# Performance work log

Hardware: AMD Instinct MI355X
Metric: run time of the kernel (lower is better)

## Reference

```python
import jax, jax.numpy as jnp
import numpy as np

ALPHA = 0.25        # focal alpha
GAMMA = 2.0         # focal gamma
POS_T = 0.5         # max_iou positive threshold
NEG_T = 0.4         # max_iou negative threshold
SL1_BETA = 1.0 / 9.0  # smooth_l1 with sigma=3
EPS = 1e-6

N, T, A, C = 8, 64, 65536, 80


def setup_inputs() -> dict:
    key = jax.random.key(0)
    ks = jax.random.split(key, 6)
    labels = jax.random.randint(ks[0], (N, T), 1, C)
    y_true = jax.nn.one_hot(labels, C, dtype=jnp.float32)
    xy = jax.random.uniform(ks[1], (N, T, 2)) * 0.7
    wh = jax.random.uniform(ks[2], (N, T, 2)) * 0.25 + 0.02
    bbox_true = jnp.concatenate([xy, xy + wh], axis=-1)
    valid = (jnp.arange(T) < 24).astype(jnp.float32)  # zero-pad remaining GT rows
    bbox_true = bbox_true * valid[None, :, None]
    axy = jax.random.uniform(ks[3], (A, 2)) * 0.9
    awh = jax.random.uniform(jax.random.fold_in(ks[3], 1), (A, 2)) * 0.15 + 0.02
    anchors = jnp.concatenate([axy, axy + awh], axis=-1)
    y_pred = jax.random.normal(ks[4], (N, A, C), dtype=jnp.float32)
    bbox_pred = jax.random.normal(ks[5], (N, A, 4), dtype=jnp.float32) * 0.1
    return {"y_true": y_true, "bbox_true": bbox_true, "y_pred": y_pred,
            "bbox_pred": bbox_pred, "anchors": anchors}


def _iou(b1, b2):
    # b1: (T,4), b2: (A,4) -> (T,A)
    a1 = jnp.maximum(b1[:, 2] - b1[:, 0], 0) * jnp.maximum(b1[:, 3] - b1[:, 1], 0)
    a2 = jnp.maximum(b2[:, 2] - b2[:, 0], 0) * jnp.maximum(b2[:, 3] - b2[:, 1], 0)
    lt = jnp.maximum(b1[:, None, :2], b2[None, :, :2])
    rb = jnp.minimum(b1[:, None, 2:], b2[None, :, 2:])
    wh = jnp.maximum(rb - lt, 0.0)
    inter = wh[..., 0] * wh[..., 1]
    union = a1[:, None] + a2[None, :] - inter
    return inter / jnp.maximum(union, 1e-10)


def _bbox2delta(boxes, anchors):
    # standard (dx, dy, dw, dh) encoding, mean=0 / std=1
    wa = jnp.maximum(anchors[:, 2] - anchors[:, 0], EPS)
    ha = jnp.maximum(anchors[:, 3] - anchors[:, 1], EPS)
    cxa = anchors[:, 0] + 0.5 * wa
    cya = anchors[:, 1] + 0.5 * ha
    wt = jnp.maximum(boxes[:, 2] - boxes[:, 0], EPS)
    ht = jnp.maximum(boxes[:, 3] - boxes[:, 1], EPS)
    cxt = boxes[:, 0] + 0.5 * (boxes[:, 2] - boxes[:, 0])
    cyt = boxes[:, 1] + 0.5 * (boxes[:, 3] - boxes[:, 1])
    return jnp.stack([(cxt - cxa) / wa, (cyt - cya) / ha,
                      jnp.log(wt / wa), jnp.log(ht / ha)], axis=-1)


def _encode_target(y_true_i, bbox_true_i, anchors):
    # y_true_i: (T,C), bbox_true_i: (T,4), anchors: (A,4)
    valid = jnp.any(bbox_true_i > 0, axis=-1)                 # (T,)
    iou = jnp.where(valid[:, None], _iou(bbox_true_i, anchors), -1.0)  # (T,A)
    max_iou = iou.max(axis=0)                                  # (A,)
    assigned = iou.argmax(axis=0)                              # (A,) gt index per anchor
    pos = max_iou >= POS_T
    neg = (max_iou < NEG_T)
    # low-quality matching: each valid gt's best anchor is positive for that gt
    gt_best = iou.argmax(axis=1)                               # (T,)
    gt_best_iou = iou.max(axis=1)
    lq = valid & (gt_best_iou > 0)
    assigned = assigned.at[gt_best].set(jnp.where(lq, jnp.arange(bbox_true_i.shape[0]), assigned[gt_best]))
    pos = pos.at[gt_best].set(jnp.where(lq, True, pos[gt_best]))
    neg = neg & (~pos)
    state = jnp.where(pos, 1, jnp.where(neg, -1, 0)).astype(jnp.int8)[:, None]  # (A,1)
    # class target: background one-hot [1,0,...,0], positives get gt label
    bg = jnp.zeros((anchors.shape[0], y_true_i.shape[-1]), jnp.float32).at[:, 0].set(1.0)
    yt = jnp.where(pos[:, None], y_true_i[assigned], bg)       # (A,C)
    delta = _bbox2delta(bbox_true_i[assigned], anchors)        # (A,4)
    bt = jnp.where(pos[:, None], delta, 0.0)
    return state, yt, bt


def _focal_bce(y_true, logits):
    # elementwise sigmoid focal loss
    ce = jnp.maximum(logits, 0) - logits * y_true + jnp.log1p(jnp.exp(-jnp.abs(logits)))
    p = jax.nn.sigmoid(logits)
    p_t = y_true * p + (1.0 - y_true) * (1.0 - p)
    a_t = y_true * ALPHA + (1.0 - y_true) * (1.0 - ALPHA)
    return a_t * jnp.power(1.0 - p_t, GAMMA) * ce


def _smooth_l1(y_true, y_pred):
    d = jnp.abs(y_true - y_pred)
    return jnp.where(d < SL1_BETA, 0.5 * d * d / SL1_BETA, d - 0.5 * SL1_BETA)


def _sanitize(x):
    return jnp.where(jnp.isnan(x) | jnp.isinf(x), 0.0, x)


def reference(y_true, bbox_true, y_pred, bbox_pred, anchors):
    state, yt, bt = jax.vmap(lambda a, b: _encode_target(a, b, anchors))(y_true, bbox_true)
    positive_w = (state == 1).astype(y_pred.dtype)   # (N,A,1)
    target_w = (state != 0).astype(y_pred.dtype)     # (N,A,1)
    avg_factor = jnp.sum(jnp.maximum(jnp.sum(positive_w, axis=-2), 1.0))
    yt = yt * positive_w                              # background=False zeroes non-positives
    cls = jnp.sum(_focal_bce(yt, y_pred) * target_w) / avg_factor
    box = jnp.sum(_smooth_l1(bt, bbox_pred) * positive_w) / avg_factor
    return _sanitize(cls), _sanitize(box)
```

## Files before the change

kernel.cpp:

```cpp
#include <hip/hip_runtime.h>
#include <hip/hip_bf16.h>
#include <math.h>

#define NB 8
#define TB 64
#define AB 65536
#define CB 80
#define EPSF 1e-6f

#define LOSS_BLOCKS 2048
#define LOSS_ITERS  16

#define WS_LABEL_OFF  4096
#define WS_CODE_OFF   8192
#define WS_PCLS_OFF   (WS_CODE_OFF + NB*AB*4)
#define WS_PBOX_OFF   (WS_PCLS_OFF + LOSS_BLOCKS*4)
#define WS_PPOS_OFF   (WS_PBOX_OFF + LOSS_BLOCKS*4)

__device__ __forceinline__ float focal0(float l) {
    float u  = __expf(l);
    float r  = __builtin_amdgcn_rcpf(1.f + u);
    float p  = 1.f - r;
    float lg = __log2f(r);
    return p * p * lg * -0.5198603854f;
}
__device__ __forceinline__ float focal_diff(float l) {
    float u  = __expf(l);
    float r  = __builtin_amdgcn_rcpf(1.f + u);
    float p  = 1.f - r;
    float sp = -0.6931471806f * __log2f(r);
    float f1 = 0.25f * r * r * (sp - l);
    float f0 = 0.75f * p * p * sp;
    return f1 - f0;
}
__device__ __forceinline__ float smooth_l1(float x) {
    float d = fabsf(x);
    return d < (1.f / 9.f) ? 4.5f * d * d : d - (0.5f / 9.f);
}

__global__ __launch_bounds__(256) void assign_kernel(
    const float* __restrict__ bbox_true,
    const float* __restrict__ anchors,
    int*   __restrict__ code,
    unsigned long long* __restrict__ gt_key)
{
    __shared__ float4 s_box[TB];
    __shared__ float  s_a1[TB];
    __shared__ unsigned long long s_key[TB];

    const int blk   = blockIdx.x;
    const int i     = blk >> 8;
    const int abase = (blk & 255) << 8;
    const int tid   = threadIdx.x;

    if (tid < TB) {
        float4 b = ((const float4*)bbox_true)[i * TB + tid];
        s_box[tid] = b;
        s_a1[tid]  = fmaxf(b.z - b.x, 0.f) * fmaxf(b.w - b.y, 0.f);
        s_key[tid] = 0ull;
    }
    __syncthreads();

    const int a = abase + tid;
    const float4 an = ((const float4*)anchors)[a];
    const float a2 = fmaxf(an.z - an.x, 0.f) * fmaxf(an.w - an.y, 0.f);

    float best = -1.0f;
    int bestt = 0;
    #pragma unroll 8
    for (int t = 0; t < TB; ++t) {
        float4 b = s_box[t];
        float lx = fmaxf(b.x, an.x), ly = fmaxf(b.y, an.y);
        float rx = fminf(b.z, an.z), ry = fminf(b.w, an.w);
        float w = fmaxf(rx - lx, 0.f), h = fmaxf(ry - ly, 0.f);
        float inter = w * h;
        float uni = s_a1[t] + a2 - inter;
        float iou = inter * __builtin_amdgcn_rcpf(fmaxf(uni, 1e-10f));
        if (iou > 0.f) {
            unsigned long long key =
                ((unsigned long long)__float_as_uint(iou) << 32) |
                (unsigned long long)((unsigned)a ^ 0xFFFFFFFFu);
            if (key > s_key[t])
                atomicMax(&s_key[t], key);
        }
        if (iou > best) { best = iou; bestt = t; }
    }
    bool pos = best >= 0.5f;
    bool neg = best < 0.4f;
    code[i * AB + a] = pos ? bestt : (neg ? -1 : -2);

    __syncthreads();
    if (tid < TB) {
        unsigned long long k = s_key[tid];
        if (k) atomicMax(&gt_key[i * TB + tid], k);
    }
}

__global__ void lq_label_kernel(const unsigned long long* __restrict__ gt_key,
                                const float* __restrict__ y_true,
                                int* __restrict__ code,
                                int* __restrict__ labels)
{
    __shared__ unsigned long long sk[NB * TB];
    const int tid = threadIdx.x;
    sk[tid] = gt_key[tid];

    const float* row = y_true + (size_t)tid * CB;
    int lab = 0;
    for (int c = 0; c < CB; ++c)
        if (row[c] > 0.5f) lab = c;
    labels[tid] = lab;

    __syncthreads();
    const int i = tid >> 6, t = tid & 63;
    unsigned long long k = sk[tid];
    if (k) {
        unsigned a = (unsigned)(k & 0xFFFFFFFFull) ^ 0xFFFFFFFFu;
        bool win = true;
        for (int t2 = t + 1; t2 < TB; ++t2) {
            unsigned long long k2 = sk[(i << 6) | t2];
            if (k2 && (((unsigned)(k2 & 0xFFFFFFFFull) ^ 0xFFFFFFFFu) == a))
                win = false;
        }
        if (win) code[i * AB + (int)a] = t;
    }
}

__global__ __launch_bounds__(320) void loss_kernel(
    const float* __restrict__ bbox_true,
    const float* __restrict__ y_pred,
    const float* __restrict__ bbox_pred,
    const float* __restrict__ anchors,
    const int*   __restrict__ code,
    const int*   __restrict__ labels,
    float* __restrict__ partial_cls,
    float* __restrict__ partial_box,
    int*   __restrict__ partial_pos)
{
    const int tid   = threadIdx.x;
    const int la    = tid / 20;
    const int chunk = tid % 20;
    const int b   = blockIdx.x;
    const int i   = b >> 8;
    const int sub = b & 255;

    const float4* yp4 = (const float4*)y_pred;

    float cls_acc = 0.f, box_acc = 0.f;
    int posc = 0;

    #pragma unroll 2
    for (int it = 0; it < LOSS_ITERS; ++it) {
        const int a = sub * 16 + la + it * (256 * 16);
        const int g = i * AB + a;
        const int cv = code[g];
        float4 l4 = yp4[g * 20 + chunk];
        if (cv != -2) {
            cls_acc += focal0(l4.x) + focal0(l4.y) + focal0(l4.z) + focal0(l4.w);
            if (cv >= 0) {
                int lab = labels[i * TB + cv];
                if (chunk == (lab >> 2)) {
                    int e = lab & 3;
                    float le = (e == 0) ? l4.x : (e == 1) ? l4.y
                             : (e == 2) ? l4.z : l4.w;
                    cls_acc += focal_diff(le);
                }
                if (chunk == 0) {
                    posc += 1;
                    float4 bt = ((const float4*)bbox_true)[i * TB + cv];
                    float4 an = ((const float4*)anchors)[a];
                    float wa = fmaxf(an.z - an.x, EPSF), ha = fmaxf(an.w - an.y, EPSF);
                    float cxa = an.x + 0.5f * wa,  cya = an.y + 0.5f * ha;
                    float wt = fmaxf(bt.z - bt.x, EPSF), ht = fmaxf(bt.w - bt.y, EPSF);
                    float cxt = bt.x + 0.5f * (bt.z - bt.x);
                    float cyt = bt.y + 0.5f * (bt.w - bt.y);
                    float d0 = (cxt - cxa) / wa, d1 = (cyt - cya) / ha;
                    float d2 = __logf(wt / wa),  d3 = __logf(ht / ha);
                    float4 bp = ((const float4*)bbox_pred)[g];
                    box_acc += smooth_l1(d0 - bp.x) + smooth_l1(d1 - bp.y) +
                               smooth_l1(d2 - bp.z) + smooth_l1(d3 - bp.w);
                }
            }
        }
    }

    for (int off = 32; off > 0; off >>= 1) {
        cls_acc += __shfl_down(cls_acc, off);
        box_acc += __shfl_down(box_acc, off);
        posc    += __shfl_down(posc, off);
    }
    __shared__ float s_cls[5], s_box[5];
    __shared__ int   s_pc[5];
    int wave = tid >> 6, lane = tid & 63;
    if (lane == 0) { s_cls[wave] = cls_acc; s_box[wave] = box_acc; s_pc[wave] = posc; }
    __syncthreads();
    if (tid == 0) {
        partial_cls[b] = s_cls[0] + s_cls[1] + s_cls[2] + s_cls[3] + s_cls[4];
        partial_box[b] = s_box[0] + s_box[1] + s_box[2] + s_box[3] + s_box[4];
        partial_pos[b] = s_pc[0] + s_pc[1] + s_pc[2] + s_pc[3] + s_pc[4];
    }
}

__global__ __launch_bounds__(256) void reduce_kernel(
    const float* __restrict__ partial_cls,
    const float* __restrict__ partial_box,
    const int*   __restrict__ partial_pos,
    float* __restrict__ out)
{
    const int tid = threadIdx.x;
    const int wave = tid >> 6, lane = tid & 63;
    __shared__ double sc[4], sb[4];
    __shared__ int    si[4];
    __shared__ float  s_avg;

    double c = 0.0, bx = 0.0;
    #pragma unroll
    for (int j = 0; j < LOSS_BLOCKS / 256; ++j) {
        c  += (double)partial_cls[tid + j * 256];
        bx += (double)partial_box[tid + j * 256];
    }

    float avg = 0.f;
    for (int bb = 0; bb < NB; ++bb) {
        int p = partial_pos[bb * 256 + tid];
        for (int off = 32; off > 0; off >>= 1) p += __shfl_down(p, off);
        if (lane == 0) si[wave] = p;
        __syncthreads();
        if (tid == 0) {
            int tot = si[0] + si[1] + si[2] + si[3];
            avg += fmaxf((float)tot, 1.0f);
        }
        __syncthreads();
    }
    if (tid == 0) s_avg = avg;

    for (int off = 32; off > 0; off >>= 1) {
        c  += __shfl_down(c, off);
        bx += __shfl_down(bx, off);
    }
    if (lane == 0) { sc[wave] = c; sb[wave] = bx; }
    __syncthreads();
    if (tid == 0) {
        double ct = sc[0] + sc[1] + sc[2] + sc[3];
        double bt = sb[0] + sb[1] + sb[2] + sb[3];
        float cf = (float)(ct / (double)s_avg);
        float bf = (float)(bt / (double)s_avg);
        if (isnan(cf) || isinf(cf)) cf = 0.f;
        if (isnan(bf) || isinf(bf)) bf = 0.f;
        out[0] = cf;
        out[1] = bf;
    }
}

extern "C" void kernel_launch(void* const* d_in, const int* in_sizes, int n_in,
                              void* d_out, int out_size, void* d_ws, size_t ws_size,
                              hipStream_t stream) {
    const float* y_true    = (const float*)d_in[0];
    const float* bbox_true = (const float*)d_in[1];
    const float* y_pred    = (const float*)d_in[2];
    const float* bbox_pred = (const float*)d_in[3];
    const float* anchors   = (const float*)d_in[4];
    float* out = (float*)d_out;

    char* ws = (char*)d_ws;
    unsigned long long* gt_key = (unsigned long long*)ws;
    int*   labels  = (int*)(ws + WS_LABEL_OFF);
    int*   code    = (int*)(ws + WS_CODE_OFF);
    float* p_cls   = (float*)(ws + WS_PCLS_OFF);
    float* p_box   = (float*)(ws + WS_PBOX_OFF);
    int*   p_pos   = (int*)(ws + WS_PPOS_OFF);

    hipMemsetAsync(ws, 0, 4096, stream);

    assign_kernel<<<NB * AB / 256, 256, 0, stream>>>(bbox_true, anchors, code, gt_key);
    lq_label_kernel<<<1, NB * TB, 0, stream>>>(gt_key, y_true, code, labels);
    loss_kernel<<<LOSS_BLOCKS, 320, 0, stream>>>(
        bbox_true, y_pred, bbox_pred, anchors, code, labels,
        p_cls, p_box, p_pos);
    reduce_kernel<<<1, 256, 0, stream>>>(p_cls, p_box, p_pos, out);
}
```

Measured before the change: 308.4 us.

## Replace per-anchor atomic GT-best tracking with dedicated per-GT reduction kernel

Removes the shared-memory and global 64-bit atomicMax used to find each ground truth's best anchor inside the assign kernel. A new gtbest kernel runs one block per GT box, scans all anchors, and reduces with shuffles, skipping zero-padded GT rows. Because every key is now written directly, the workspace memset is dropped. The loss kernel also applies the ignore mask as a multiply instead of a branch and unrolls deeper. This adds a second full IoU pass over the anchors and one more kernel launch.

```diff
diff --git a/kernel.cpp b/kernel.cpp
--- a/kernel.cpp
+++ b/kernel.cpp
@@ -41,12 +41,10 @@
 __global__ __launch_bounds__(256) void assign_kernel(
     const float* __restrict__ bbox_true,
     const float* __restrict__ anchors,
-    int*   __restrict__ code,
-    unsigned long long* __restrict__ gt_key)
+    int*   __restrict__ code)
 {
     __shared__ float4 s_box[TB];
     __shared__ float  s_a1[TB];
-    __shared__ unsigned long long s_key[TB];
 
     const int blk   = blockIdx.x;
     const int i     = blk >> 8;
@@ -57,7 +55,6 @@
         float4 b = ((const float4*)bbox_true)[i * TB + tid];
         s_box[tid] = b;
         s_a1[tid]  = fmaxf(b.z - b.x, 0.f) * fmaxf(b.w - b.y, 0.f);
-        s_key[tid] = 0ull;
     }
     __syncthreads();
 
@@ -76,23 +73,55 @@
         float inter = w * h;
         float uni = s_a1[t] + a2 - inter;
         float iou = inter * __builtin_amdgcn_rcpf(fmaxf(uni, 1e-10f));
-        if (iou > 0.f) {
-            unsigned long long key =
-                ((unsigned long long)__float_as_uint(iou) << 32) |
-                (unsigned long long)((unsigned)a ^ 0xFFFFFFFFu);
-            if (key > s_key[t])
-                atomicMax(&s_key[t], key);
-        }
         if (iou > best) { best = iou; bestt = t; }
     }
     bool pos = best >= 0.5f;
     bool neg = best < 0.4f;
     code[i * AB + a] = pos ? bestt : (neg ? -1 : -2);
-
-    __syncthreads();
-    if (tid < TB) {
-        unsigned long long k = s_key[tid];
-        if (k) atomicMax(&gt_key[i * TB + tid], k);
+}
+
+__global__ __launch_bounds__(512) void gtbest_kernel(
+    const float* __restrict__ bbox_true,
+    const float* __restrict__ anchors,
+    unsigned long long* __restrict__ gt_key)
+{
+    const int bt  = blockIdx.x;
+    const int tid = threadIdx.x;
+    const float4 b = ((const float4*)bbox_true)[bt];
+    const bool valid = (b.x > 0.f) || (b.y > 0.f) || (b.z > 0.f) || (b.w > 0.f);
+    const float a1 = fmaxf(b.z - b.x, 0.f) * fmaxf(b.w - b.y, 0.f);
+
+    unsigned long long best = 0ull;
+    if (valid) {
+        for (int a = tid; a < AB; a += 512) {
+            float4 an = ((const float4*)anchors)[a];
+            float a2 = fmaxf(an.z - an.x, 0.f) * fmaxf(an.w - an.y, 0.f);
+            float lx = fmaxf(b.x, an.x), ly = fmaxf(b.y, an.y);
+            float rx = fminf(b.z, an.z), ry = fminf(b.w, an.w);
+            float w = fmaxf(rx - lx, 0.f), h = fmaxf(ry - ly, 0.f);
+            float inter = w * h;
+            float uni = a1 + a2 - inter;
+            float iou = inter * __builtin_amdgcn_rcpf(fmaxf(uni, 1e-10f));
+            unsigned long long key = (iou > 0.f)
+                ? (((unsigned long long)__float_as_uint(iou) << 32) |
+                   (unsigned long long)((unsigned)a ^ 0xFFFFFFFFu))
+                : 0ull;
+            best = (key > best) ? key : best;
+        }
+    }
+    for (int off = 32; off > 0; off >>= 1) {
+        unsigned long long o = __shfl_down(best, off);
+        best = (o > best) ? o : best;
+    }
+    __shared__ unsigned long long sk[8];
+    int wave = tid >> 6, lane = tid & 63;
+    if (lane == 0) sk[wave] = best;
+    __syncthreads();
+    if (tid == 0) {
+        unsigned long long m = sk[0];
+        #pragma unroll
+        for (int wv = 1; wv < 8; ++wv) m = (sk[wv] > m) ? sk[wv] : m;
+        gt_key[bt] = m;
     }
 }
 
@@ -140,46 +169,45 @@
     const int tid   = threadIdx.x;
     const int la    = tid / 20;
     const int chunk = tid % 20;
-    const int b   = blockIdx.x;
-    const int i   = b >> 8;
-    const int sub = b & 255;
+    const int blk = blockIdx.x;
+    const int i   = blk >> 8;
+    const int sub = blk & 255;
 
     const float4* yp4 = (const float4*)y_pred;
 
     float cls_acc = 0.f, box_acc = 0.f;
     int posc = 0;
 
-    #pragma unroll 2
+    #pragma unroll 4
     for (int it = 0; it < LOSS_ITERS; ++it) {
         const int a = sub * 16 + la + it * (256 * 16);
         const int g = i * AB + a;
         const int cv = code[g];
         float4 l4 = yp4[g * 20 + chunk];
-        if (cv != -2) {
-            cls_acc += focal0(l4.x) + focal0(l4.y) + focal0(l4.z) + focal0(l4.w);
-            if (cv >= 0) {
-                int lab = labels[i * TB + cv];
-                if (chunk == (lab >> 2)) {
-                    int e = lab & 3;
-                    float le = (e == 0) ? l4.x : (e == 1) ? l4.y
-                             : (e == 2) ? l4.z : l4.w;
-                    cls_acc += focal_diff(le);
-                }
-                if (chunk == 0) {
-                    posc += 1;
-                    float4 bt = ((const float4*)bbox_true)[i * TB + cv];
-                    float4 an = ((const float4*)anchors)[a];
-                    float wa = fmaxf(an.z - an.x, EPSF), ha = fmaxf(an.w - an.y, EPSF);
-                    float cxa = an.x + 0.5f * wa,  cya = an.y + 0.5f * ha;
-                    float wt = fmaxf(bt.z - bt.x, EPSF), ht = fmaxf(bt.w - bt.y, EPSF);
-                    float cxt = bt.x + 0.5f * (bt.z - bt.x);
-                    float cyt = bt.y + 0.5f * (bt.w - bt.y);
-                    float d0 = (cxt - cxa) / wa, d1 = (cyt - cya) / ha;
-                    float d2 = __logf(wt / wa),  d3 = __logf(ht / ha);
-                    float4 bp = ((const float4*)bbox_pred)[g];
-                    box_acc += smooth_l1(d0 - bp.x) + smooth_l1(d1 - bp.y) +
-                               smooth_l1(d2 - bp.z) + smooth_l1(d3 - bp.w);
-                }
+        float m = (cv != -2) ? 1.f : 0.f;
+        cls_acc += m * (focal0(l4.x) + focal0(l4.y) + focal0(l4.z) + focal0(l4.w));
+        if (cv >= 0) {
+            int lab = labels[i * TB + cv];
+            if (chunk == (lab >> 2)) {
+                int e = lab & 3;
+                float le = (e == 0) ? l4.x : (e == 1) ? l4.y
+                         : (e == 2) ? l4.z : l4.w;
+                cls_acc += focal_diff(le);
+            }
+            if (chunk == 0) {
+                posc += 1;
+                float4 bt = ((const float4*)bbox_true)[i * TB + cv];
+                float4 an = ((const float4*)anchors)[a];
+                float wa = fmaxf(an.z - an.x, EPSF), ha = fmaxf(an.w - an.y, EPSF);
+                float cxa = an.x + 0.5f * wa,  cya = an.y + 0.5f * ha;
+                float wt = fmaxf(bt.z - bt.x, EPSF), ht = fmaxf(bt.w - bt.y, EPSF);
+                float cxt = bt.x + 0.5f * (bt.z - bt.x);
+                float cyt = bt.y + 0.5f * (bt.w - bt.y);
+                float d0 = (cxt - cxa) / wa, d1 = (cyt - cya) / ha;
+                float d2 = __logf(wt / wa),  d3 = __logf(ht / ha);
+                float4 bp = ((const float4*)bbox_pred)[g];
+                box_acc += smooth_l1(d0 - bp.x) + smooth_l1(d1 - bp.y) +
+                           smooth_l1(d2 - bp.z) + smooth_l1(d3 - bp.w);
             }
         }
     }
@@ -195,9 +223,9 @@
     if (lane == 0) { s_cls[wave] = cls_acc; s_box[wave] = box_acc; s_pc[wave] = posc; }
     __syncthreads();
     if (tid == 0) {
-        partial_cls[b] = s_cls[0] + s_cls[1] + s_cls[2] + s_cls[3] + s_cls[4];
-        partial_box[b] = s_box[0] + s_box[1] + s_box[2] + s_box[3] + s_box[4];
-        partial_pos[b] = s_pc[0] + s_pc[1] + s_pc[2] + s_pc[3] + s_pc[4];
+        partial_cls[blk] = s_cls[0] + s_cls[1] + s_cls[2] + s_cls[3] + s_cls[4];
+        partial_box[blk] = s_box[0] + s_box[1] + s_box[2] + s_box[3] + s_box[4];
+        partial_pos[blk] = s_pc[0] + s_pc[1] + s_pc[2] + s_pc[3] + s_pc[4];
     }
 }
 
@@ -270,9 +298,9 @@
     float* p_box   = (float*)(ws + WS_PBOX_OFF);
     int*   p_pos   = (int*)(ws + WS_PPOS_OFF);
 
-    hipMemsetAsync(ws, 0, 4096, stream);
-
-    assign_kernel<<<NB * AB / 256, 256, 0, stream>>>(bbox_true, anchors, code, gt_key);
+
+    assign_kernel<<<NB * AB / 256, 256, 0, stream>>>(bbox_true, anchors, code);
+    gtbest_kernel<<<NB * TB, 512, 0, stream>>>(bbox_true, anchors, gt_key);
     lq_label_kernel<<<1, NB * TB, 0, stream>>>(gt_key, y_true, code, labels);
     loss_kernel<<<LOSS_BLOCKS, 320, 0, stream>>>(
         bbox_true, y_pred, bbox_pred, anchors, code, labels,
```

New measurement: 327.7 us. +6.3%, slower.
